# Kernel tuning notes

Measured on AMD Instinct MI355X. Metric: run time of the kernel, lower is better.

Reference implementation:

```python
import jax, jax.numpy as jnp
import numpy as np

EMBED = 4
H1, H2 = 8, 4


def setup_inputs() -> dict:
    key = jax.random.key(0)
    ks = jax.random.split(key, 10)
    x = jax.random.normal(ks[0], (1024, 256, EMBED), dtype=jnp.float32)
    Wq = jax.random.normal(ks[1], (EMBED, EMBED), dtype=jnp.float32)
    Wk = jax.random.normal(ks[2], (EMBED, EMBED), dtype=jnp.float32)
    Wv = jax.random.normal(ks[3], (EMBED, EMBED), dtype=jnp.float32)
    # nn.Linear default init: U(-1/sqrt(fan_in), 1/sqrt(fan_in)); approximate with uniform
    def lin(k, fan_in, fan_out):
        k1, k2 = jax.random.split(k)
        bound = 1.0 / np.sqrt(fan_in)
        W = jax.random.uniform(k1, (fan_in, fan_out), minval=-bound, maxval=bound, dtype=jnp.float32)
        b = jax.random.uniform(k2, (fan_out,), minval=-bound, maxval=bound, dtype=jnp.float32)
        return W, b
    W1, b1 = lin(ks[4], EMBED, H1)
    W2, b2 = lin(ks[5], H1, H2)
    W3, b3 = lin(ks[6], H2, 1)
    return {"x": x, "Wq": Wq, "Wk": Wk, "Wv": Wv,
            "W1": W1, "b1": b1, "W2": W2, "b2": b2, "W3": W3, "b3": b3}


def reference(x, Wq, Wk, Wv, W1, b1, W2, b2, W3, b3):
    # Self-attention: x [B, S, E]
    q = x @ Wq
    k = x @ Wk
    v = x @ Wv
    scale = 1.0 / np.sqrt(EMBED).astype(np.float32)
    scores = jax.nn.softmax(jnp.einsum('bse,bte->bst', q, k) * scale, axis=-1)
    attn_out = jnp.einsum('bst,bte->bse', scores, v)
    h = jnp.tanh(attn_out @ W1 + b1)
    h = jnp.tanh(h @ W2 + b2)
    return h @ W3 + b3  # [B, S, 1]
```

## Files before the change

kernel.cpp:

```cpp
#include <hip/hip_runtime.h>
#include <math.h>

constexpr int S  = 256;
constexpr int E  = 4;
constexpr int H1 = 8;
constexpr int H2 = 4;
constexpr int NW  = 4;
constexpr int NP  = S / 2;
constexpr int PPW = NP / NW;
constexpr int R   = 4;

typedef float v2f __attribute__((ext_vector_type(2)));

__device__ __forceinline__ v2f fma2(v2f a, v2f b, v2f c) {
    return __builtin_elementwise_fma(a, b, c);
}
__device__ __forceinline__ float fast_tanh(float x) {
    const float z = __builtin_amdgcn_exp2f(x * 2.88539008f);
    return 1.f - 2.f * __builtin_amdgcn_rcpf(z + 1.f);
}

__global__ __launch_bounds__(256, 4) void attn_mlp_kernel(
    const float* __restrict__ x,
    const float* __restrict__ Wq, const float* __restrict__ Wk, const float* __restrict__ Wv,
    const float* __restrict__ W1, const float* __restrict__ b1,
    const float* __restrict__ W2, const float* __restrict__ b2,
    const float* __restrict__ W3, const float* __restrict__ b3,
    float* __restrict__ out)
{
    const int b    = blockIdx.x;
    const int tid  = threadIdx.x;
    const int w    = tid >> 6;
    const int lane = tid & 63;

    __shared__ float4 q_lds[S];
    __shared__ __align__(16) float kp_lds[NP][E][2];
    __shared__ __align__(16) float vp_lds[NP][E][2];
    __shared__ float4 acc_lds[NW][S];
    __shared__ float  l_lds[NW][S];
    __shared__ float  kmax_lds[NW];

    const float4 xr = *reinterpret_cast<const float4*>(x + ((size_t)b * S + tid) * E);
    const float xv[E] = {xr.x, xr.y, xr.z, xr.w};
    {
        const int jp = tid >> 1, c = tid & 1;
        float4 q;
        float* qp = &q.x;
        float kk = 0.f;
        #pragma unroll
        for (int e = 0; e < E; ++e) {
            float aq = 0.f, ak = 0.f, av = 0.f;
            #pragma unroll
            for (int i = 0; i < E; ++i) {
                aq = fmaf(xv[i], Wq[i * E + e], aq);
                ak = fmaf(xv[i], Wk[i * E + e], ak);
                av = fmaf(xv[i], Wv[i * E + e], av);
            }
            qp[e] = aq * (0.5f * 1.44269504f);
            kp_lds[jp][e][c] = ak;
            vp_lds[jp][e][c] = av;
            kk = fmaf(ak, ak, kk);
        }
        q_lds[tid] = q;

        #pragma unroll
        for (int off = 32; off > 0; off >>= 1)
            kk = fmaxf(kk, __shfl_xor(kk, off));
        if (lane == 0) kmax_lds[w] = kk;
    }
    __syncthreads();

    const float kmax2 = fmaxf(fmaxf(kmax_lds[0], kmax_lds[1]),
                              fmaxf(kmax_lds[2], kmax_lds[3]));

    v2f qx2[R], qy2[R], qz2[R], qw2[R], mh2[R];
    #pragma unroll
    for (int rr = 0; rr < R; ++rr) {
        const float4 q = q_lds[lane + 64 * rr];
        const float qq = fmaf(q.x, q.x, fmaf(q.y, q.y, fmaf(q.z, q.z, q.w * q.w)));
        const float mh = sqrtf(qq * kmax2);
        qx2[rr] = v2f{q.x, q.x};
        qy2[rr] = v2f{q.y, q.y};
        qz2[rr] = v2f{q.z, q.z};
        qw2[rr] = v2f{q.w, q.w};
        mh2[rr] = v2f{-mh, -mh};
    }

    v2f l2[R], a0[R], a1[R], a2[R], a3[R];
    #pragma unroll
    for (int rr = 0; rr < R; ++rr) {
        l2[rr] = v2f{0.f, 0.f};
        a0[rr] = a1[rr] = a2[rr] = a3[rr] = v2f{0.f, 0.f};
    }

    const int p0 = w * PPW;
    #pragma unroll 4
    for (int jp = p0; jp < p0 + PPW; ++jp) {
        const float4* kf = reinterpret_cast<const float4*>(&kp_lds[jp][0][0]);
        const float4* vf = reinterpret_cast<const float4*>(&vp_lds[jp][0][0]);
        const float4 k01 = kf[0], k23 = kf[1];
        const float4 v01 = vf[0], v23 = vf[1];
        const v2f kx = {k01.x, k01.y}, ky = {k01.z, k01.w};
        const v2f kz = {k23.x, k23.y}, kw = {k23.z, k23.w};
        const v2f vx = {v01.x, v01.y}, vy = {v01.z, v01.w};
        const v2f vz = {v23.x, v23.y}, vw = {v23.z, v23.w};
        #pragma unroll
        for (int rr = 0; rr < R; ++rr) {
            v2f s2 = fma2(qw2[rr], kw, mh2[rr]);
            s2 = fma2(qz2[rr], kz, s2);
            s2 = fma2(qy2[rr], ky, s2);
            s2 = fma2(qx2[rr], kx, s2);
            const v2f p2 = {__builtin_amdgcn_exp2f(s2.x),
                            __builtin_amdgcn_exp2f(s2.y)};
            l2[rr] += p2;
            a0[rr] = fma2(p2, vx, a0[rr]);
            a1[rr] = fma2(p2, vy, a1[rr]);
            a2[rr] = fma2(p2, vz, a2[rr]);
            a3[rr] = fma2(p2, vw, a3[rr]);
        }
    }

    #pragma unroll
    for (int rr = 0; rr < R; ++rr) {
        const int row = lane + 64 * rr;
        acc_lds[w][row] = make_float4(a0[rr].x + a0[rr].y,
                                      a1[rr].x + a1[rr].y,
                                      a2[rr].x + a2[rr].y,
                                      a3[rr].x + a3[rr].y);
        l_lds[w][row] = l2[rr].x + l2[rr].y;
    }
    __syncthreads();

    float lsum = 0.f;
    float ax = 0.f, ay = 0.f, az = 0.f, aw = 0.f;
    #pragma unroll
    for (int ww = 0; ww < NW; ++ww) {
        lsum += l_lds[ww][tid];
        const float4 a4 = acc_lds[ww][tid];
        ax += a4.x; ay += a4.y; az += a4.z; aw += a4.w;
    }
    const float inv = 1.0f / lsum;
    const float a[E] = {ax * inv, ay * inv, az * inv, aw * inv};

    float h1[H1];
    #pragma unroll
    for (int o = 0; o < H1; ++o) {
        float s = b1[o];
        #pragma unroll
        for (int i = 0; i < E; ++i) s = fmaf(a[i], W1[i * H1 + o], s);
        h1[o] = fast_tanh(s);
    }
    float h2[H2];
    #pragma unroll
    for (int o = 0; o < H2; ++o) {
        float s = b2[o];
        #pragma unroll
        for (int i = 0; i < H1; ++i) s = fmaf(h1[i], W2[i * H2 + o], s);
        h2[o] = fast_tanh(s);
    }
    float r = b3[0];
    #pragma unroll
    for (int i = 0; i < H2; ++i) r = fmaf(h2[i], W3[i], r);

    out[(size_t)b * S + tid] = r;
}

extern "C" void kernel_launch(void* const* d_in, const int* in_sizes, int n_in,
                              void* d_out, int out_size, void* d_ws, size_t ws_size,
                              hipStream_t stream) {
    const float* x  = (const float*)d_in[0];
    const float* Wq = (const float*)d_in[1];
    const float* Wk = (const float*)d_in[2];
    const float* Wv = (const float*)d_in[3];
    const float* W1 = (const float*)d_in[4];
    const float* b1 = (const float*)d_in[5];
    const float* W2 = (const float*)d_in[6];
    const float* b2 = (const float*)d_in[7];
    const float* W3 = (const float*)d_in[8];
    const float* b3 = (const float*)d_in[9];
    float* out = (float*)d_out;

    const int B = in_sizes[0] / (S * E);
    attn_mlp_kernel<<<dim3(B), dim3(256), 0, stream>>>(
        x, Wq, Wk, Wv, W1, b1, W2, b2, W3, b3, out);
}
```

Baseline: 89.12 us.

## Move attention score and PV products onto MFMA with split-precision fp16/bf16

Replaces the scalar packed-FMA attention loop with MFMA instructions. QK^T uses fp16 hi/lo splits of q and k packed into a single 16x16x32 fragment, and PV uses bf16 hi/lo splits of probabilities and values, with a row of ones in V so the softmax denominator comes out of the same matrix product. Each wave now owns 64 query rows over all keys, so the cross-wave partial-sum reduction is gone. The intent is to offload the FMA-bound inner loop to matrix cores. In exchange it adds extra split and pack work per tile and accepts somewhat reduced precision from dropping the lo×lo terms.

Measured after the change: 88.82 us. Within noise of the previous version (-0.3%).

```diff
diff --git a/kernel.cpp b/kernel.cpp
--- a/kernel.cpp
+++ b/kernel.cpp
@@ -5,19 +5,55 @@
 constexpr int E  = 4;
 constexpr int H1 = 8;
 constexpr int H2 = 4;
-constexpr int NW  = 4;
-constexpr int NP  = S / 2;
-constexpr int PPW = NP / NW;
-constexpr int R   = 4;
-
-typedef float v2f __attribute__((ext_vector_type(2)));
-
-__device__ __forceinline__ v2f fma2(v2f a, v2f b, v2f c) {
-    return __builtin_elementwise_fma(a, b, c);
-}
+
+typedef __attribute__((ext_vector_type(8))) _Float16 half8;
+typedef __attribute__((ext_vector_type(8))) short    bf16x8;
+typedef __attribute__((ext_vector_type(4))) float    f32x4;
+typedef __attribute__((ext_vector_type(4))) int      i32x4;
+
 __device__ __forceinline__ float fast_tanh(float x) {
     const float z = __builtin_amdgcn_exp2f(x * 2.88539008f);
     return 1.f - 2.f * __builtin_amdgcn_rcpf(z + 1.f);
+}
+
+__device__ __forceinline__ void split16(float x, unsigned short& hi, unsigned short& lo) {
+    _Float16 h = (_Float16)x;
+    float r = x - (float)h;
+    _Float16 l = (_Float16)r;
+    hi = __builtin_bit_cast(unsigned short, h);
+    lo = __builtin_bit_cast(unsigned short, l);
+}
+
+__device__ __forceinline__ unsigned short bf16_rne(float x) {
+    unsigned u = __builtin_bit_cast(unsigned, x);
+    u = (u + 0x7FFFu + ((u >> 16) & 1u)) >> 16;
+    return (unsigned short)u;
+}
+__device__ __forceinline__ float bf16_as_f32(unsigned short h) {
+    return __builtin_bit_cast(float, (unsigned)h << 16);
+}
+
+__device__ __forceinline__ unsigned pk_bf16(float a, float b) {
+    return __builtin_amdgcn_perm(__builtin_bit_cast(unsigned, b),
+                                 __builtin_bit_cast(unsigned, a), 0x07060302u);
+}
+__device__ __forceinline__ float hi_part(float a) {
+    return __builtin_bit_cast(float, __builtin_bit_cast(unsigned, a) & 0xFFFF0000u);
+}
+
+__device__ __forceinline__ half8 frag(int a, int b, int c, int d) {
+    i32x4 t = {a, b, c, d};
+    return __builtin_bit_cast(half8, t);
+}
+__device__ __forceinline__ bf16x8 bfrag(int a, int b, int c, int d) {
+    i32x4 t = {a, b, c, d};
+    return __builtin_bit_cast(bf16x8, t);
+}
+__device__ __forceinline__ f32x4 mfma_f16(half8 a, half8 b, f32x4 c) {
+    return __builtin_amdgcn_mfma_f32_16x16x32_f16(a, b, c, 0, 0, 0);
+}
+__device__ __forceinline__ f32x4 mfma_bf16(bf16x8 a, bf16x8 b, f32x4 c) {
+    return __builtin_amdgcn_mfma_f32_16x16x32_bf16(a, b, c, 0, 0, 0);
 }
 
 __global__ __launch_bounds__(256, 4) void attn_mlp_kernel(
@@ -32,21 +68,22 @@
     const int tid  = threadIdx.x;
     const int w    = tid >> 6;
     const int lane = tid & 63;
-
-    __shared__ float4 q_lds[S];
-    __shared__ __align__(16) float kp_lds[NP][E][2];
-    __shared__ __align__(16) float vp_lds[NP][E][2];
-    __shared__ float4 acc_lds[NW][S];
-    __shared__ float  l_lds[NW][S];
-    __shared__ float  kmax_lds[NW];
+    const int g    = lane >> 4;
+    const int c15  = lane & 15;
+
+    __shared__ i32x4 qrec[S];
+    __shared__ i32x4 krec[S];
+    __shared__ __align__(16) unsigned short vhT[16][264];
+    __shared__ __align__(16) unsigned short vlT[16][264];
+    __shared__ float mh_lds[S];
+    __shared__ float accb[S][9];
+    __shared__ float kmax_lds[4];
 
     const float4 xr = *reinterpret_cast<const float4*>(x + ((size_t)b * S + tid) * E);
     const float xv[E] = {xr.x, xr.y, xr.z, xr.w};
+    float qq = 0.f, kk = 0.f;
     {
-        const int jp = tid >> 1, c = tid & 1;
-        float4 q;
-        float* qp = &q.x;
-        float kk = 0.f;
+        float q[E], k[E], v[E];
         #pragma unroll
         for (int e = 0; e < E; ++e) {
             float aq = 0.f, ak = 0.f, av = 0.f;
@@ -56,12 +93,34 @@
                 ak = fmaf(xv[i], Wk[i * E + e], ak);
                 av = fmaf(xv[i], Wv[i * E + e], av);
             }
-            qp[e] = aq * (0.5f * 1.44269504f);
-            kp_lds[jp][e][c] = ak;
-            vp_lds[jp][e][c] = av;
+            q[e] = aq * 0.72134752f;
+            k[e] = ak;
+            v[e] = av;
+            qq = fmaf(q[e], q[e], qq);
             kk = fmaf(ak, ak, kk);
         }
-        q_lds[tid] = q;
+        unsigned short qh[4], ql[4], kh[4], kl[4];
+        #pragma unroll
+        for (int e = 0; e < E; ++e) {
+            split16(q[e], qh[e], ql[e]);
+            split16(k[e], kh[e], kl[e]);
+        }
+        qrec[tid] = (i32x4){ (int)(qh[0] | (qh[1] << 16)), (int)(qh[2] | (qh[3] << 16)),
+                             (int)(ql[0] | (ql[1] << 16)), (int)(ql[2] | (ql[3] << 16)) };
+        krec[tid] = (i32x4){ (int)(kh[0] | (kh[1] << 16)), (int)(kh[2] | (kh[3] << 16)),
+                             (int)(kl[0] | (kl[1] << 16)), (int)(kl[2] | (kl[3] << 16)) };
+        #pragma unroll
+        for (int e = 0; e < E; ++e) {
+            const unsigned short vh = bf16_rne(v[e]);
+            const unsigned short vl = bf16_rne(v[e] - bf16_as_f32(vh));
+            vhT[e][tid] = vh;
+            vlT[e][tid] = vl;
+        }
+        vhT[4][tid] = 0x3F80;
+        #pragma unroll
+        for (int r = 5; r < 16; ++r) vhT[r][tid] = 0;
+        #pragma unroll
+        for (int r = 4; r < 16; ++r) vlT[r][tid] = 0;
 
         #pragma unroll
         for (int off = 32; off > 0; off >>= 1)
@@ -69,98 +128,106 @@
         if (lane == 0) kmax_lds[w] = kk;
     }
     __syncthreads();
-
     const float kmax2 = fmaxf(fmaxf(kmax_lds[0], kmax_lds[1]),
                               fmaxf(kmax_lds[2], kmax_lds[3]));
-
-    v2f qx2[R], qy2[R], qz2[R], qw2[R], mh2[R];
-    #pragma unroll
-    for (int rr = 0; rr < R; ++rr) {
-        const float4 q = q_lds[lane + 64 * rr];
-        const float qq = fmaf(q.x, q.x, fmaf(q.y, q.y, fmaf(q.z, q.z, q.w * q.w)));
-        const float mh = sqrtf(qq * kmax2);
-        qx2[rr] = v2f{q.x, q.x};
-        qy2[rr] = v2f{q.y, q.y};
-        qz2[rr] = v2f{q.z, q.z};
-        qw2[rr] = v2f{q.w, q.w};
-        mh2[rr] = v2f{-mh, -mh};
-    }
-
-    v2f l2[R], a0[R], a1[R], a2[R], a3[R];
-    #pragma unroll
-    for (int rr = 0; rr < R; ++rr) {
-        l2[rr] = v2f{0.f, 0.f};
-        a0[rr] = a1[rr] = a2[rr] = a3[rr] = v2f{0.f, 0.f};
-    }
-
-    const int p0 = w * PPW;
-    #pragma unroll 4
-    for (int jp = p0; jp < p0 + PPW; ++jp) {
-        const float4* kf = reinterpret_cast<const float4*>(&kp_lds[jp][0][0]);
-        const float4* vf = reinterpret_cast<const float4*>(&vp_lds[jp][0][0]);
-        const float4 k01 = kf[0], k23 = kf[1];
-        const float4 v01 = vf[0], v23 = vf[1];
-        const v2f kx = {k01.x, k01.y}, ky = {k01.z, k01.w};
-        const v2f kz = {k23.x, k23.y}, kw = {k23.z, k23.w};
-        const v2f vx = {v01.x, v01.y}, vy = {v01.z, v01.w};
-        const v2f vz = {v23.x, v23.y}, vw = {v23.z, v23.w};
-        #pragma unroll
-        for (int rr = 0; rr < R; ++rr) {
-            v2f s2 = fma2(qw2[rr], kw, mh2[rr]);
-            s2 = fma2(qz2[rr], kz, s2);
-            s2 = fma2(qy2[rr], ky, s2);
-            s2 = fma2(qx2[rr], kx, s2);
-            const v2f p2 = {__builtin_amdgcn_exp2f(s2.x),
-                            __builtin_amdgcn_exp2f(s2.y)};
-            l2[rr] += p2;
-            a0[rr] = fma2(p2, vx, a0[rr]);
-            a1[rr] = fma2(p2, vy, a1[rr]);
-            a2[rr] = fma2(p2, vz, a2[rr]);
-            a3[rr] = fma2(p2, vw, a3[rr]);
-        }
-    }
-
-    #pragma unroll
-    for (int rr = 0; rr < R; ++rr) {
-        const int row = lane + 64 * rr;
-        acc_lds[w][row] = make_float4(a0[rr].x + a0[rr].y,
-                                      a1[rr].x + a1[rr].y,
-                                      a2[rr].x + a2[rr].y,
-                                      a3[rr].x + a3[rr].y);
-        l_lds[w][row] = l2[rr].x + l2[rr].y;
-    }
+    mh_lds[tid] = -sqrtf(qq * kmax2);
     __syncthreads();
 
-    float lsum = 0.f;
-    float ax = 0.f, ay = 0.f, az = 0.f, aw = 0.f;
-    #pragma unroll
-    for (int ww = 0; ww < NW; ++ww) {
-        lsum += l_lds[ww][tid];
-        const float4 a4 = acc_lds[ww][tid];
-        ax += a4.x; ay += a4.y; az += a4.z; aw += a4.w;
-    }
-    const float inv = 1.0f / lsum;
-    const float a[E] = {ax * inv, ay * inv, az * inv, aw * inv};
-
-    float h1[H1];
+    half8 Bq[4];
+    float negmh[4];
+    f32x4 acc[4];
+    #pragma unroll
+    for (int rt = 0; rt < 4; ++rt) {
+        const int s = 64 * w + 16 * rt + c15;
+        i32x4 u = qrec[s];
+        int h0 = (g == 0) ? u[0] : u[2];
+        int h1 = (g == 0) ? u[1] : u[3];
+        if (g >= 2) { h0 = 0; h1 = 0; }
+        Bq[rt] = frag(h0, h1, h0, h1);
+        negmh[rt] = mh_lds[s];
+        acc[rt] = (f32x4){0.f, 0.f, 0.f, 0.f};
+    }
+
+    #pragma unroll 1
+    for (int ch = 0; ch < 8; ++ch) {
+        const int kb = ch * 32;
+        i32x4 k0 = krec[kb + c15];
+        i32x4 k1 = krec[kb + 16 + c15];
+        if (g >= 2) { k0 = (i32x4){0,0,0,0}; k1 = (i32x4){0,0,0,0}; }
+        const half8 Ak0 = __builtin_bit_cast(half8, k0);
+        const half8 Ak1 = __builtin_bit_cast(half8, k1);
+
+        const int vi = kb + 4 * g;
+        const uint2 h0 = *(const uint2*)&vhT[c15][vi];
+        const uint2 h1 = *(const uint2*)&vhT[c15][vi + 16];
+        const uint2 l0 = *(const uint2*)&vlT[c15][vi];
+        const uint2 l1 = *(const uint2*)&vlT[c15][vi + 16];
+        const bf16x8 Bvh0 = bfrag((int)h0.x, (int)h0.y, (int)h0.x, (int)h0.y);
+        const bf16x8 Bvh1 = bfrag((int)h1.x, (int)h1.y, (int)h1.x, (int)h1.y);
+        const bf16x8 Bvl  = bfrag((int)l0.x, (int)l0.y, (int)l1.x, (int)l1.y);
+
+        #pragma unroll
+        for (int rt = 0; rt < 4; ++rt) {
+            const f32x4 cm = {negmh[rt], negmh[rt], negmh[rt], negmh[rt]};
+            const f32x4 c0 = mfma_f16(Ak0, Bq[rt], cm);
+            const f32x4 c1 = mfma_f16(Ak1, Bq[rt], cm);
+            const float p0 = __builtin_amdgcn_exp2f(c0[0]);
+            const float p1 = __builtin_amdgcn_exp2f(c0[1]);
+            const float p2 = __builtin_amdgcn_exp2f(c0[2]);
+            const float p3 = __builtin_amdgcn_exp2f(c0[3]);
+            const float p4 = __builtin_amdgcn_exp2f(c1[0]);
+            const float p5 = __builtin_amdgcn_exp2f(c1[1]);
+            const float p6 = __builtin_amdgcn_exp2f(c1[2]);
+            const float p7 = __builtin_amdgcn_exp2f(c1[3]);
+            const unsigned hi01 = pk_bf16(p0, p1), hi23 = pk_bf16(p2, p3);
+            const unsigned hi45 = pk_bf16(p4, p5), hi67 = pk_bf16(p6, p7);
+            const unsigned lo01 = pk_bf16(p0 - hi_part(p0), p1 - hi_part(p1));
+            const unsigned lo23 = pk_bf16(p2 - hi_part(p2), p3 - hi_part(p3));
+            const unsigned lo45 = pk_bf16(p4 - hi_part(p4), p5 - hi_part(p5));
+            const unsigned lo67 = pk_bf16(p6 - hi_part(p6), p7 - hi_part(p7));
+            const bf16x8 A10 = bfrag((int)hi01, (int)hi23, (int)lo01, (int)lo23);
+            const bf16x8 A11 = bfrag((int)hi45, (int)hi67, (int)lo45, (int)lo67);
+            const bf16x8 A2  = bfrag((int)hi01, (int)hi23, (int)hi45, (int)hi67);
+            acc[rt] = mfma_bf16(A10, Bvh0, acc[rt]);
+            acc[rt] = mfma_bf16(A11, Bvh1, acc[rt]);
+            acc[rt] = mfma_bf16(A2,  Bvl,  acc[rt]);
+        }
+    }
+
+    #pragma unroll
+    for (int rt = 0; rt < 4; ++rt) {
+        if (c15 < 5) {
+            const int row = 64 * w + 16 * rt + 4 * g;
+            #pragma unroll
+            for (int i = 0; i < 4; ++i) accb[row + i][c15] = acc[rt][i];
+        }
+    }
+    __syncthreads();
+
+    const float inv = 1.0f / fmaxf(accb[tid][4], 1e-37f);
+    float a[E];
+    #pragma unroll
+    for (int e = 0; e < E; ++e) a[e] = accb[tid][e] * inv;
+
+    float h1v[H1];
     #pragma unroll
     for (int o = 0; o < H1; ++o) {
         float s = b1[o];
         #pragma unroll
         for (int i = 0; i < E; ++i) s = fmaf(a[i], W1[i * H1 + o], s);
-        h1[o] = fast_tanh(s);
-    }
-    float h2[H2];
+        h1v[o] = fast_tanh(s);
+    }
+    float h2v[H2];
     #pragma unroll
     for (int o = 0; o < H2; ++o) {
         float s = b2[o];
         #pragma unroll
-        for (int i = 0; i < H1; ++i) s = fmaf(h1[i], W2[i * H2 + o], s);
-        h2[o] = fast_tanh(s);
+        for (int i = 0; i < H1; ++i) s = fmaf(h1v[i], W2[i * H2 + o], s);
+        h2v[o] = fast_tanh(s);
     }
     float r = b3[0];
     #pragma unroll
-    for (int i = 0; i < H2; ++i) r = fmaf(h2[i], W3[i], r);
+    for (int i = 0; i < H2; ++i) r = fmaf(h2v[i], W3[i], r);
 
     out[(size_t)b * S + tid] = r;
 }
```
